# Kernel optimization log

Hardware: AMD Instinct MI355X
Metric: run time of the kernel (lower is better)

## Reference

```python
import jax, jax.numpy as jnp
from jax import lax
import numpy as np

GRID_SIZE = 8
MARGIN = 1.0
NUM_NEG = 16
SOS_NEG = 8
LOSS_LAMBDA = 1.0
B, N, C = 2, 512, 128
H = W = 128  # descriptor map; image is GRID_SIZE*H = 1024


def dist_matrix(a, b):
    # Euclidean cdist for 2-D points; exact 0 for identical rows (needed for <=1e-8 tests).
    d = a[:, :, None, :] - b[:, None, :, :]
    # distances only feed topk indices / boolean masks -> no grad path (matches torch)
    return lax.stop_gradient(jnp.sqrt(jnp.sum(d * d, axis=-1)))


def inv_sim_matrix(d1, d2):
    return 2.0 - 2.0 * jnp.einsum('bnc,bmc->bnm', d1, d2)


def inv_sim_vector(d1, d2):
    return 2.0 - 2.0 * jnp.sum(d1 * d2, axis=-1)


def make_coo_grid(h, w, gs, b):
    ys = gs * jnp.arange(h, dtype=jnp.float32) + gs / 2.0
    xs = gs * jnp.arange(w, dtype=jnp.float32) + gs / 2.0
    g = jnp.stack(jnp.meshgrid(ys, xs, indexing='ij'), axis=-1)  # H W 2 (y, x)
    return jnp.broadcast_to(g.reshape(1, h * w, 2), (b, h * w, 2))


def warp_points(p, Hm):
    xy = p[..., ::-1]  # (y,x) -> (x,y)
    ph = jnp.concatenate([xy, jnp.ones_like(xy[..., :1])], axis=-1)
    wp = jnp.einsum('bij,bmj->bmi', Hm, ph)
    wp = wp[..., :2] / (wp[..., 2:3] + 1e-8)
    return wp[..., ::-1]  # back to (y,x)


def sample_descriptors(desc, kp, gs):
    # bilinear sample of desc (B,C,H,W) at image-space keypoints (y,x), then L2-normalize
    b, c, h, w = desc.shape
    y = jnp.clip(kp[..., 0] / gs - 0.5, 0.0, h - 1.0)
    x = jnp.clip(kp[..., 1] / gs - 0.5, 0.0, w - 1.0)
    y0 = jnp.clip(jnp.floor(y), 0, h - 2).astype(jnp.int32)
    x0 = jnp.clip(jnp.floor(x), 0, w - 2).astype(jnp.int32)
    wy = (y - y0)[..., None]
    wx = (x - x0)[..., None]
    dmap = desc.transpose(0, 2, 3, 1).reshape(b, h * w, c)
    def g(yi, xi):
        idx = jnp.broadcast_to((yi * w + xi)[..., None], yi.shape + (c,))
        return jnp.take_along_axis(dmap, idx, axis=1)
    v = (g(y0, x0) * (1 - wy) * (1 - wx) + g(y0, x0 + 1) * (1 - wy) * wx
         + g(y0 + 1, x0) * wy * (1 - wx) + g(y0 + 1, x0 + 1) * wy * wx)
    return v / (jnp.linalg.norm(v, axis=-1, keepdims=True) + 1e-8)


def take2(coo, idx):
    # gather 2-D points: coo (B,M,2), idx (B,K) -> (B,K,2)
    return jnp.take_along_axis(coo, jnp.broadcast_to(idx[:, :, None], idx.shape + (2,)), axis=1)


def smallest_k(x, k):
    vals, ids = lax.top_k(-x, k)
    return -vals, ids


def setup_inputs() -> dict:
    key = jax.random.key(0)
    k1, k2, k3, k4, k5 = jax.random.split(key, 5)
    img = float(GRID_SIZE * H)
    kp1 = jax.random.uniform(k1, (B, N, 2), dtype=jnp.float32) * (img - 1.0)
    w_kp1 = jax.random.uniform(k2, (B, N, 2), dtype=jnp.float32) * (img - 1.0)
    d = jax.random.normal(k3, (B, N, C), dtype=jnp.float32)
    kp1_desc = d / jnp.linalg.norm(d, axis=-1, keepdims=True)
    desc2 = jax.random.normal(k4, (B, C, H, W), dtype=jnp.float32)
    homo12 = jnp.broadcast_to(jnp.eye(3, dtype=jnp.float32), (B, 3, 3)) \
        + 1e-3 * jax.random.normal(k5, (B, 3, 3), dtype=jnp.float32)
    return {'kp1': kp1, 'w_kp1': w_kp1, 'kp1_desc': kp1_desc, 'desc2': desc2, 'homo12': homo12}


def reference(kp1, w_kp1, kp1_desc, desc2, homo12):
    b, n, c = kp1_desc.shape
    _, _, h, w = desc2.shape
    hw = h * w
    gs = GRID_SIZE

    w_kp1_desc = sample_descriptors(desc2, w_kp1, gs)  # b n c
    pos = inv_sim_vector(kp1_desc, w_kp1_desc)  # b n
    pos = jnp.repeat(pos[:, :, None], NUM_NEG, axis=2).reshape(b, n * NUM_NEG)

    coo = make_coo_grid(h, w, gs, b)  # b hw 2
    kp1_cell_ids = smallest_k(dist_matrix(kp1, coo), 4)[1].reshape(b, 4 * n)
    kp1_cells = take2(coo, kp1_cell_ids)  # b 4n 2
    kp1_w_cells = warp_points(kp1_cells, homo12)
    kp1_w_cell_cell_ids = smallest_k(dist_matrix(kp1_w_cells, coo), 4)[1]  # b 4n 4

    bb = jnp.arange(b)[:, None, None]
    rr = jnp.arange(4 * n)[None, :, None]
    neigh = jnp.zeros((b, 4 * n, hw), jnp.float32).at[bb, rr, kp1_w_cell_cell_ids].set(1.0)
    neigh = neigh.reshape(b, n, 4, hw).sum(axis=2)  # b n hw

    desc2f = desc2.transpose(0, 2, 3, 1).reshape(b, hw, c)
    dsim = inv_sim_matrix(kp1_desc, desc2f) + neigh * 5.0
    neg = smallest_k(dsim, NUM_NEG)[0].reshape(b, n * NUM_NEG)
    fos = jnp.mean(jnp.maximum(pos - neg + MARGIN, 0.0) ** 2) * LOSS_LAMBDA

    cc = dist_matrix(kp1_cells, kp1_cells)  # b 4n 4n
    kp1_mask = (cc <= 1e-8).reshape(b, n, 4, n, 4).sum(-1).sum(2).astype(jnp.float32)  # b n n

    kp1_w_cell_cells = take2(coo, kp1_w_cell_cell_ids.reshape(b, 16 * n))  # b 16n 2
    w_ids = smallest_k(dist_matrix(w_kp1, coo), 4)[1].reshape(b, 4 * n)
    w_kp1_cells = take2(coo, w_ids)  # b 4n 2
    d4 = dist_matrix(kp1_w_cell_cells, w_kp1_cells)  # b 16n 4n
    w_kp1_mask = (d4 <= 1e-8).reshape(b, n, 4, 4, n, 4).sum(-1).sum(3).sum(2).astype(jnp.float32)

    k_sim = inv_sim_matrix(kp1_desc, kp1_desc) + kp1_mask * 5.0
    w_sim = inv_sim_matrix(w_kp1_desc, w_kp1_desc) + w_kp1_mask * 5.0
    k_neg_ids = smallest_k(k_sim, SOS_NEG)[1].reshape(b, n * SOS_NEG)
    w_neg_ids = smallest_k(w_sim, SOS_NEG)[1].reshape(b, n * SOS_NEG)

    def gatherC(x, idx):
        return jnp.take_along_axis(x, jnp.broadcast_to(idx[:, :, None], idx.shape + (c,)), axis=1)
    k_neg_desc = gatherC(kp1_desc, k_neg_ids)
    w_neg_desc = gatherC(w_kp1_desc, w_neg_ids)
    k_rep = jnp.repeat(kp1_desc[:, :, None, :], SOS_NEG, axis=2).reshape(b, n * SOS_NEG, c)
    w_rep = jnp.repeat(w_kp1_desc[:, :, None, :], SOS_NEG, axis=2).reshape(b, n * SOS_NEG, c)

    sos_v = inv_sim_vector(k_rep, k_neg_desc) - inv_sim_vector(w_rep, w_neg_desc)
    sos = jnp.mean(jnp.sqrt(jnp.sum((sos_v ** 2).reshape(b, n, SOS_NEG), axis=-1)))
    return (fos + sos) * LOSS_LAMBDA
```

## Files before the change

### kernel.cpp

```cpp
#include <hip/hip_runtime.h>
#include <climits>

#define B_ 2
#define N_ 512
#define C_ 128
#define H_ 128
#define W_ 128
#define HW_ (H_ * W_)
#define NUM_NEG_ 16
#define SOS_NEG_ 8
#define SCAP_ 128

typedef __attribute__((ext_vector_type(8))) short short8;
typedef __attribute__((ext_vector_type(4))) float f32x4;

__device__ inline unsigned int f2bf(float x) {
    unsigned int u = __float_as_uint(x);
    return (u + 0x7FFFu + ((u >> 16) & 1u)) >> 16;
}
__device__ inline float bf2f(unsigned int h) {
    return __uint_as_float(h << 16);
}

__device__ inline void nearest4(float y, float x, int out[4]) {
// ... 150 lines not shown
        s += __shfl_xor(s, 1);  s += __shfl_xor(s, 2);  s += __shfl_xor(s, 4);
        s += __shfl_xor(s, 8);  s += __shfl_xor(s, 16); s += __shfl_xor(s, 32);
        float inv = 1.0f / (sqrtf(s) + 1e-8f);
        float vn0 = v0 * inv, vn1 = v1 * inv;
        w_bf[(size_t)bn * C_ + l]      = (unsigned short)f2bf(vn0);
        w_bf[(size_t)bn * C_ + 64 + l] = (unsigned short)f2bf(vn1);
        float qd0 = kp1_desc[(size_t)bn * C_ + l];
        float qd1 = kp1_desc[(size_t)bn * C_ + 64 + l];
        float d = qd0 * vn0 + qd1 * vn1;
        d += __shfl_xor(d, 1);  d += __shfl_xor(d, 2);  d += __shfl_xor(d, 4);
        d += __shfl_xor(d, 8);  d += __shfl_xor(d, 16); d += __shfl_xor(d, 32);
        if (l == 0) pos[bn] = 2.0f - 2.0f * d;
    }
}

__global__ __launch_bounds__(512) void hqt_kb(
    const unsigned short* __restrict__ q_bf,
    const unsigned short* __restrict__ w_bf,
    const unsigned short* __restrict__ d2t,
    const int* __restrict__ cid4, const int* __restrict__ wid4,
    const int* __restrict__ wcc16,
    float* __restrict__ rowmax, float* __restrict__ psim) {
    int blk = blockIdx.x;
    int tid = threadIdx.x, w = tid >> 6, l = tid & 63;
    int l15 = l & 15, lg = l >> 4;
    if (blk < 256) {
        int b = blk >> 7;
        int rg = (blk >> 4) & 7;
        int cb = blk & 15;
        int rowbase = rg * 64;
        int colbase = cb * 1024 + w * 128;
        const unsigned short* qb = q_bf + (size_t)b * N_ * C_;
        const unsigned short* db = d2t + (size_t)b * HW_ * C_;
        short8 a[4][4];
#pragma unroll
        for (int rt = 0; rt < 4; ++rt)
#pragma unroll
            for (int ks = 0; ks < 4; ++ks)
                a[rt][ks] = *(const short8*)(qb + (size_t)(rowbase + rt * 16 + l15) * C_ + ks * 32 + lg * 8);
        f32x4 mx[4];
#pragma unroll
        for (int rt = 0; rt < 4; ++rt) mx[rt] = f32x4{-1e30f, -1e30f, -1e30f, -1e30f};
#pragma unroll
        for (int t = 0; t < 8; ++t) {
            const unsigned short* dp = db + (size_t)(colbase + t * 16 + l15) * C_ + lg * 8;
            short8 b0 = *(const short8*)(dp);
            short8 b1 = *(const short8*)(dp + 32);
            short8 b2 = *(const short8*)(dp + 64);
            short8 b3 = *(const short8*)(dp + 96);
#pragma unroll
            for (int rt = 0; rt < 4; ++rt) {
                f32x4 acc4 = {0.0f, 0.0f, 0.0f, 0.0f};
                acc4 = __builtin_amdgcn_mfma_f32_16x16x32_bf16(a[rt][0], b0, acc4, 0, 0, 0);
                acc4 = __builtin_amdgcn_mfma_f32_16x16x32_bf16(a[rt][1], b1, acc4, 0, 0, 0);
                acc4 = __builtin_amdgcn_mfma_f32_16x16x32_bf16(a[rt][2], b2, acc4, 0, 0, 0);
                acc4 = __builtin_amdgcn_mfma_f32_16x16x32_bf16(a[rt][3], b3, acc4, 0, 0, 0);
#pragma unroll
                for (int r = 0; r < 4; ++r) mx[rt][r] = fmaxf(mx[rt][r], acc4[r]);
            }
        }
#pragma unroll
        for (int rt = 0; rt < 4; ++rt)
#pragma unroll
            for (int r = 0; r < 4; ++r) {
                float v = mx[rt][r];
                v = fmaxf(v, __shfl_xor(v, 1));
                v = fmaxf(v, __shfl_xor(v, 2));
                v = fmaxf(v, __shfl_xor(v, 4));
                v = fmaxf(v, __shfl_xor(v, 8));
                mx[rt][r] = v;
            }
        if (l15 == 0) {
            int chunk = cb * 8 + w;
#pragma unroll
            for (int rt = 0; rt < 4; ++rt)
#pragma unroll
                for (int r = 0; r < 4; ++r) {
                    int rowg = b * N_ + rowbase + rt * 16 + lg * 4 + r;
                    rowmax[(size_t)rowg * 128 + chunk] = mx[rt][r];
                }
        }
    } else {
        int blk2 = blk - 256;
        int mat = blk2 >> 6;
        int b = (blk2 >> 5) & 1;
        int r0 = (blk2 & 31) * 16;
        const unsigned short* src = (mat ? w_bf : q_bf) + (size_t)b * N_ * C_;

        __shared__ int s_colids[N_][4];
        __shared__ int s_rowcc[16][16];
        {
            const int4* gsrc = (const int4*)((mat ? wid4 : cid4) + b * N_ * 4);
            ((int4*)s_colids)[tid] = gsrc[tid];
            if (tid < 256)
                ((int*)s_rowcc)[tid] = wcc16[(b * N_ + r0) * 16 + tid];
        }
        short8 a0 = *(const short8*)(src + (size_t)(r0 + l15) * C_ + lg * 8);
        short8 a1 = *(const short8*)(src + (size_t)(r0 + l15) * C_ + 32 + lg * 8);
        short8 a2 = *(const short8*)(src + (size_t)(r0 + l15) * C_ + 64 + lg * 8);
        short8 a3 = *(const short8*)(src + (size_t)(r0 + l15) * C_ + 96 + lg * 8);
        __syncthreads();

        int4 rowc[4];
        int rcc[4][16];
#pragma unroll
        for (int r = 0; r < 4; ++r) {
            rowc[r] = *(const int4*)(&s_colids[r0 + lg * 4 + r][0]);
            if (mat == 1) {
#pragma unroll
                for (int i = 0; i < 16; ++i) rcc[r][i] = s_rowcc[lg * 4 + r][i];
            }
        }

        float* prow = psim + ((size_t)(mat * B_ + b) * N_) * N_;
#pragma unroll
        for (int t = 0; t < 4; ++t) {
            int col0 = w * 64 + t * 16;
            const unsigned short* dp = src + (size_t)(col0 + l15) * C_ + lg * 8;
            short8 b0 = *(const short8*)(dp);
            short8 b1 = *(const short8*)(dp + 32);
            short8 b2 = *(const short8*)(dp + 64);
            short8 b3 = *(const short8*)(dp + 96);
            f32x4 acc4 = {0.0f, 0.0f, 0.0f, 0.0f};
            acc4 = __builtin_amdgcn_mfma_f32_16x16x32_bf16(a0, b0, acc4, 0, 0, 0);
            acc4 = __builtin_amdgcn_mfma_f32_16x16x32_bf16(a1, b1, acc4, 0, 0, 0);
            acc4 = __builtin_amdgcn_mfma_f32_16x16x32_bf16(a2, b2, acc4, 0, 0, 0);
            acc4 = __builtin_amdgcn_mfma_f32_16x16x32_bf16(a3, b3, acc4, 0, 0, 0);
            int mycol = col0 + l15;
            int4 cc = *(const int4*)(&s_colids[mycol][0]);
#pragma unroll
            for (int r = 0; r < 4; ++r) {
                int cnt = 0;
                if (mat == 0) {
#pragma unroll
                    for (int j = 0; j < 4; ++j) {
                        int u = (j == 0) ? rowc[r].x : (j == 1) ? rowc[r].y
                              : (j == 2) ? rowc[r].z : rowc[r].w;
                        cnt += (u == cc.x) + (u == cc.y) + (u == cc.z) + (u == cc.w);
                    }
                } else {
#pragma unroll
                    for (int i = 0; i < 16; ++i) {
                        int u = rcc[r][i];
                        cnt += (u == cc.x) + (u == cc.y) + (u == cc.z) + (u == cc.w);
                    }
                }
                float key = acc4[r] - 2.5f * (float)cnt;
                prow[(size_t)(r0 + lg * 4 + r) * N_ + mycol] = key;
            }
        }
    }
}

__global__ __launch_bounds__(256) void hqt_k3b(
    const float* __restrict__ rowmax, float* __restrict__ t32) {
    int w = threadIdx.x >> 6, l = threadIdx.x & 63;
    int row = blockIdx.x * 4 + w;
    const float* rm = rowmax + (size_t)row * 128;
    float v = fmaxf(rm[l], rm[64 + l]);
    float t = -1e30f;
#pragma unroll 1
    for (int it = 0; it < 32; ++it) {
        float m = v;
        m = fmaxf(m, __shfl_xor(m, 1));
        m = fmaxf(m, __shfl_xor(m, 2));
        m = fmaxf(m, __shfl_xor(m, 4));
        m = fmaxf(m, __shfl_xor(m, 8));
        m = fmaxf(m, __shfl_xor(m, 16));
        m = fmaxf(m, __shfl_xor(m, 32));
        v = (v == m) ? -1e30f : v;
        t = m;
    }
    if (l == 0) t32[row] = t;
}

__global__ __launch_bounds__(512) void hqt_kc(
    const unsigned short* __restrict__ q_bf,
    const unsigned short* __restrict__ d2t,
    const float* __restrict__ t32,
    int* __restrict__ scnt, float2* __restrict__ sbuf) {
    int blk = blockIdx.x;
    int b = blk >> 7;
    int rg = (blk >> 4) & 7;
    int cb = blk & 15;
    int tid = threadIdx.x, w = tid >> 6, l = tid & 63;
    int l15 = l & 15, lg = l >> 4;
    int rowbase = rg * 64;
    int colbase = cb * 1024 + w * 128;
    const unsigned short* qb = q_bf + (size_t)b * N_ * C_;
    const unsigned short* db = d2t + (size_t)b * HW_ * C_;
    short8 a[4][4];
#pragma unroll
    for (int rt = 0; rt < 4; ++rt)
#pragma unroll
        for (int ks = 0; ks < 4; ++ks)
            a[rt][ks] = *(const short8*)(qb + (size_t)(rowbase + rt * 16 + l15) * C_ + ks * 32 + lg * 8);
    float tl[4][4];
#pragma unroll
    for (int rt = 0; rt < 4; ++rt)
#pragma unroll
        for (int r = 0; r < 4; ++r)
            tl[rt][r] = t32[b * N_ + rowbase + rt * 16 + lg * 4 + r];
#pragma unroll
    for (int t = 0; t < 8; ++t) {
        const unsigned short* dp = db + (size_t)(colbase + t * 16 + l15) * C_ + lg * 8;
        short8 b0 = *(const short8*)(dp);
        short8 b1 = *(const short8*)(dp + 32);
        short8 b2 = *(const short8*)(dp + 64);
        short8 b3 = *(const short8*)(dp + 96);
#pragma unroll
        for (int rt = 0; rt < 4; ++rt) {
            f32x4 acc4 = {0.0f, 0.0f, 0.0f, 0.0f};
            acc4 = __builtin_amdgcn_mfma_f32_16x16x32_bf16(a[rt][0], b0, acc4, 0, 0, 0);
            acc4 = __builtin_amdgcn_mfma_f32_16x16x32_bf16(a[rt][1], b1, acc4, 0, 0, 0);
            acc4 = __builtin_amdgcn_mfma_f32_16x16x32_bf16(a[rt][2], b2, acc4, 0, 0, 0);
            acc4 = __builtin_amdgcn_mfma_f32_16x16x32_bf16(a[rt][3], b3, acc4, 0, 0, 0);
#pragma unroll
            for (int r = 0; r < 4; ++r) {
                float d = acc4[r];
                if (d >= tl[rt][r]) {
                    int rowg = b * N_ + rowbase + rt * 16 + lg * 4 + r;
                    int idx = atomicAdd(scnt + rowg, 1);
                    if (idx < SCAP_) {
                        float2 e;
                        e.x = d;
                        e.y = __int_as_float(colbase + t * 16 + l15);
                        sbuf[(size_t)rowg * SCAP_ + idx] = e;
                    }
                }
            }
        }
    }
}

__device__ inline void insert8_vi(float (&av)[8], int (&ai)[8], float v, int id) {
    bool le = (v < av[7]) || (v == av[7] && id < ai[7]);
    if (!le) return;
#pragma unroll
    for (int k = 0; k < 8; ++k) {
        float ov = av[k]; int oi = ai[k];
        bool sm = (v < ov) || (v == ov && id < oi);
        av[k] = sm ? v : ov;  ai[k] = sm ? id : oi;
        v = sm ? ov : v;      id = sm ? oi : id;
    }
}

__device__ inline void bitonic8_pairs(float (&av)[8], int (&ai)[8]) {
#pragma unroll
    for (int dd = 0; dd < 3; ++dd) {
        const int d = 4 >> dd;
#pragma unroll
        for (int i = 0; i < 8; ++i) {
            if ((i & d) == 0) {
                bool sw = (av[i + d] < av[i]) ||
                          (av[i + d] == av[i] && ai[i + d] < ai[i]);
                float tv = av[i]; int ti = ai[i];
                av[i]     = sw ? av[i + d] : av[i];
                ai[i]     = sw ? ai[i + d] : ai[i];
                av[i + d] = sw ? tv : av[i + d];
                ai[i + d] = sw ? ti : ai[i + d];
            }
        }
    }
}

__device__ inline void wave_merge8(float (&av)[8], int (&ai)[8], int l) {
#pragma unroll
    for (int step = 32; step >= 1; step >>= 1) {
        float bv[8]; int bi2[8];
#pragma unroll
        for (int i = 0; i < 8; ++i) {
            bv[i]  = __shfl(av[7 - i], (l + step) & 63);
            bi2[i] = __shfl(ai[7 - i], (l + step) & 63);
        }
        bool upd = l < step;
#pragma unroll
        for (int i = 0; i < 8; ++i) {
            bool sm = (bv[i] < av[i]) || (bv[i] == av[i] && bi2[i] < ai[i]);
            if (upd && sm) { av[i] = bv[i]; ai[i] = bi2[i]; }
        }
        bitonic8_pairs(av, ai);
    }
}

__global__ __launch_bounds__(256) void hqt_kd(
    const unsigned short* __restrict__ q_bf,
    const unsigned short* __restrict__ d2t,
    const unsigned int* __restrict__ marked,
    const int* __restrict__ scnt, const float2* __restrict__ sbuf,
    const float* __restrict__ pos, const float* __restrict__ psim,
    const int* __restrict__ cid4, const int* __restrict__ wid4,
    const int* __restrict__ wcc16, float* __restrict__ acc,
    float* __restrict__ out) {
    int blk = blockIdx.x;
    int w = threadIdx.x >> 6, l = threadIdx.x & 63;
    if (blk < 256) {
        int row = blk * 4 + w;
        int b = row >> 9;
        int sc = scnt[row]; if (sc > SCAP_) sc = SCAP_;
        float k0 = -1e30f, k1 = -1e30f, k2c = -1e30f;
        int c0 = -1, c1 = -1;
        if (l < sc) {
            float2 e = sbuf[(size_t)row * SCAP_ + l];
            k0 = e.x; c0 = __float_as_int(e.y);
        }
        if (64 + l < sc) {
            float2 e = sbuf[(size_t)row * SCAP_ + 64 + l];
            k1 = e.x; c1 = __float_as_int(e.y);
        }
#pragma unroll
        for (int i = 0; i < 16; ++i) {
            unsigned int mv = marked[row * 16 + i];
            int id = (int)(mv & 0xFFFFu);
            if (c0 == id) k0 = -1e30f;
            if (c1 == id) k1 = -1e30f;
        }
        {
            int mi = l >> 2, cq = l & 3;
            unsigned int mv = marked[row * 16 + mi];
            bool valid = (mv != 0xFFFFFFFFu);
            int col = valid ? (int)(mv & 0xFFFFu) : 0;
            int cnt = (int)(mv >> 16);
            const unsigned short* qp = q_bf + (size_t)row * C_ + cq * 32;
            const unsigned short* dp = d2t + ((size_t)b * HW_ + col) * C_ + cq * 32;
            float dot = 0.0f;
#pragma unroll
            for (int u = 0; u < 4; ++u) {
                short8 qv = *(const short8*)(qp + u * 8);
                short8 dv = *(const short8*)(dp + u * 8);
#pragma unroll
                for (int e = 0; e < 8; ++e)
                    dot = fmaf(bf2f((unsigned short)qv[e]), bf2f((unsigned short)dv[e]), dot);
            }
            dot += __shfl_xor(dot, 1);
            dot += __shfl_xor(dot, 2);
            k2c = (valid && cq == 0) ? (dot - 2.5f * (float)cnt) : -1e30f;
        }
        float pos_r = pos[row];
        float sum = 0.0f;
#pragma unroll 1
        for (int it = 0; it < 16; ++it) {
            float v = fmaxf(k0, fmaxf(k1, k2c));
            float m = v;
            m = fmaxf(m, __shfl_xor(m, 1));
            m = fmaxf(m, __shfl_xor(m, 2));
            m = fmaxf(m, __shfl_xor(m, 4));
            m = fmaxf(m, __shfl_xor(m, 8));
            m = fmaxf(m, __shfl_xor(m, 16));
            m = fmaxf(m, __shfl_xor(m, 32));
            unsigned long long b0 = __ballot(k0 == m);
            if (b0) {
                if (l == __ffsll(b0) - 1) k0 = -1e30f;
            } else {
                unsigned long long b1 = __ballot(k1 == m);
                if (b1) {
                    if (l == __ffsll(b1) - 1) k1 = -1e30f;
                } else {
                    unsigned long long b2 = __ballot(k2c == m);
                    if (l == __ffsll(b2) - 1) k2c = -1e30f;
                }
            }
            float h = pos_r + 2.0f * m - 1.0f;
            h = fmaxf(h, 0.0f);
            sum += h * h;
        }
        if (l == 0) atomicAdd(acc + 0, sum);
    } else {
        int rowg = (blk - 256) * 4 + w;
        int b = rowg >> 9;
        int row = rowg & 511;

        __shared__ float s_kv[4][8], s_wv[4][8];
        __shared__ int   s_ki[4][8], s_wi[4][8];

        float kv[8]; int ki[8];
#pragma unroll
        for (int i = 0; i < 8; ++i) { kv[i] = 1e30f; ki[i] = INT_MAX; }
        {
            const float* pk = psim + ((size_t)(0 * B_ + b) * N_ + row) * N_;
            float4 u0 = ((const float4*)pk)[l * 2];
            float4 u1 = ((const float4*)pk)[l * 2 + 1];
            insert8_vi(kv, ki, -u0.x, l * 8 + 0);
            insert8_vi(kv, ki, -u0.y, l * 8 + 1);
            insert8_vi(kv, ki, -u0.z, l * 8 + 2);
            insert8_vi(kv, ki, -u0.w, l * 8 + 3);
            insert8_vi(kv, ki, -u1.x, l * 8 + 4);
            insert8_vi(kv, ki, -u1.y, l * 8 + 5);
            insert8_vi(kv, ki, -u1.z, l * 8 + 6);
            insert8_vi(kv, ki, -u1.w, l * 8 + 7);
        }
        wave_merge8(kv, ki, l);
        if (l == 0) {
#pragma unroll
            for (int i = 0; i < 8; ++i) { s_kv[w][i] = -kv[i]; s_ki[w][i] = ki[i]; }
        }

        float wv[8]; int wi[8];
#pragma unroll
        for (int i = 0; i < 8; ++i) { wv[i] = 1e30f; wi[i] = INT_MAX; }
        {
            const float* pw = psim + ((size_t)(1 * B_ + b) * N_ + row) * N_;
            float4 u0 = ((const float4*)pw)[l * 2];
            float4 u1 = ((const float4*)pw)[l * 2 + 1];
            insert8_vi(wv, wi, -u0.x, l * 8 + 0);
            insert8_vi(wv, wi, -u0.y, l * 8 + 1);
            insert8_vi(wv, wi, -u0.z, l * 8 + 2);
            insert8_vi(wv, wi, -u0.w, l * 8 + 3);
            insert8_vi(wv, wi, -u1.x, l * 8 + 4);
            insert8_vi(wv, wi, -u1.y, l * 8 + 5);
            insert8_vi(wv, wi, -u1.z, l * 8 + 6);
            insert8_vi(wv, wi, -u1.w, l * 8 + 7);
        }
        wave_merge8(wv, wi, l);
        if (l == 0) {
#pragma unroll
            for (int i = 0; i < 8; ++i) { s_wv[w][i] = -wv[i]; s_wi[w][i] = wi[i]; }
        }

        if (l < 8) {
            int kidx = s_ki[w][l]; float kkey = s_kv[w][l];
            int widx = s_wi[w][l]; float wkey = s_wv[w][l];
            const int4* cb  = (const int4*)(cid4 + b * N_ * 4);
            const int4* wb4 = (const int4*)(wid4 + b * N_ * 4);
            int4 rc = cb[row];
            int4 mc = cb[kidx];
            int cntK = 0;
#pragma unroll
            for (int j = 0; j < 4; ++j) {
                int u = (j == 0) ? rc.x : (j == 1) ? rc.y : (j == 2) ? rc.z : rc.w;
                cntK += (u == mc.x) + (u == mc.y) + (u == mc.z) + (u == mc.w);
            }
            int4 mw = wb4[widx];
            int cntW = 0;
            const int4* rcc = (const int4*)(wcc16 + (b * N_ + row) * 16);
#pragma unroll
            for (int uq = 0; uq < 4; ++uq) {
                int4 rr = rcc[uq];
                cntW += (rr.x == mw.x) + (rr.x == mw.y) + (rr.x == mw.z) + (rr.x == mw.w);
                cntW += (rr.y == mw.x) + (rr.y == mw.y) + (rr.y == mw.z) + (rr.y == mw.w);
                cntW += (rr.z == mw.x) + (rr.z == mw.y) + (rr.z == mw.z) + (rr.z == mw.w);
                cntW += (rr.w == mw.x) + (rr.w == mw.y) + (rr.w == mw.z) + (rr.w == mw.w);
            }
            float dotK = kkey + 2.5f * (float)cntK;
            float dotW = wkey + 2.5f * (float)cntW;
            float t2 = 2.0f * (dotW - dotK);
            float sq = t2 * t2;
            sq += __shfl_xor(sq, 1);
            sq += __shfl_xor(sq, 2);
            sq += __shfl_xor(sq, 4);
            if (l == 0) atomicAdd(acc + 1, sqrtf(sq));
        }
    }
    __syncthreads();
    if (threadIdx.x == 0) {
        __threadfence();
        unsigned int t = atomicAdd((unsigned int*)(acc + 2), 1u);
        if (t == 511u) {
            float a0 = atomicAdd(acc + 0, 0.0f);
            float a1 = atomicAdd(acc + 1, 0.0f);
            out[0] = a0 * (1.0f / (float)(B_ * N_ * NUM_NEG_))
                   + a1 * (1.0f / (float)(B_ * N_));
        }
    }
}

__global__ void hqt_k1_cells(const float* __restrict__ kp1,
                             const float* __restrict__ w_kp1,
                             const float* __restrict__ homo,
                             int* __restrict__ cid4,
                             int* __restrict__ wcc16,
                             int* __restrict__ wid4) {
    int t = blockIdx.x * blockDim.x + threadIdx.x;
    if (t >= B_ * N_) return;
    int b = t / N_;
    float ky = kp1[2 * t], kx = kp1[2 * t + 1];
    int ids[4];
    nearest4(ky, kx, ids);
    const float* Hb = homo + 9 * b;
    float h00 = Hb[0], h01 = Hb[1], h02 = Hb[2];
    float h10 = Hb[3], h11 = Hb[4], h12 = Hb[5];
    float h20 = Hb[6], h21 = Hb[7], h22 = Hb[8];
#pragma unroll
    for (int i = 0; i < 4; ++i) {
        int id = ids[i];
        cid4[4 * t + i] = id;
        float cy = 8.0f * (id >> 7) + 4.0f;
        float cx = 8.0f * (id & 127) + 4.0f;
        float X = cx, Y = cy;
        float wz = h20 * X + h21 * Y + h22;
        float inv = 1.0f / (wz + 1e-8f);
        float wy = (h10 * X + h11 * Y + h12) * inv;
        float wx = (h00 * X + h01 * Y + h02) * inv;
        int wids[4];
        nearest4(wy, wx, wids);
#pragma unroll
        for (int j = 0; j < 4; ++j) wcc16[16 * t + 4 * i + j] = wids[j];
    }
    float zy = w_kp1[2 * t], zx = w_kp1[2 * t + 1];
    int wi4[4];
    nearest4(zy, zx, wi4);
#pragma unroll
    for (int j = 0; j < 4; ++j) wid4[4 * t + j] = wi4[j];
}

__global__ __launch_bounds__(128) void hqt_k2_sample_f32(
    const float* __restrict__ w_kp1, const float* __restrict__ desc2,
    const float* __restrict__ kp1_desc, float* __restrict__ w_desc,
    float* __restrict__ pos) {
    int bn = blockIdx.x;
    int b = bn / N_;
    int c = threadIdx.x;
    float ky = w_kp1[2 * bn], kx = w_kp1[2 * bn + 1];
    float y = fminf(fmaxf(ky * 0.125f - 0.5f, 0.0f), (float)(H_ - 1));
    float x = fminf(fmaxf(kx * 0.125f - 0.5f, 0.0f), (float)(W_ - 1));
    int y0 = (int)floorf(y); if (y0 > H_ - 2) y0 = H_ - 2;
    int x0 = (int)floorf(x); if (x0 > W_ - 2) x0 = W_ - 2;
    float wy = y - (float)y0, wx = x - (float)x0;
    const float* dB = desc2 + ((size_t)b * C_ + c) * HW_;
    int i00 = y0 * W_ + x0;
    float v = dB[i00]          * (1.0f - wy) * (1.0f - wx)
            + dB[i00 + 1]      * (1.0f - wy) * wx
            + dB[i00 + W_]     * wy * (1.0f - wx)
            + dB[i00 + W_ + 1] * wy * wx;
    __shared__ float red[128];
    red[c] = v * v;
    __syncthreads();
    for (int s = 64; s > 0; s >>= 1) {
        if (c < s) red[c] += red[c + s];
        __syncthreads();
    }
    float nrm = sqrtf(red[0]);
    __syncthreads();
    float vn = v / (nrm + 1e-8f);
    w_desc[(size_t)bn * C_ + c] = vn;
    float qd = kp1_desc[(size_t)bn * C_ + c];
    red[c] = qd * vn;
    __syncthreads();
    for (int s = 64; s > 0; s >>= 1) {
        if (c < s) red[c] += red[c + s];
        __syncthreads();
    }
    if (c == 0) pos[bn] = 2.0f - 2.0f * red[0];
}

__device__ inline void bitonic16_asc(float (&a)[16]) {
#pragma unroll
    for (int dd = 0; dd < 4; ++dd) {
        const int d = 8 >> dd;
#pragma unroll
        for (int i = 0; i < 16; ++i) {
            if ((i & d) == 0) {
                float lo = fminf(a[i], a[i + d]);
                float hi = fmaxf(a[i], a[i + d]);
                a[i] = lo; a[i + d] = hi;
            }
        }
    }
}

#define T3 512
#define R3 4
__global__ __launch_bounds__(T3) void hqt_k3_dsim(
    const float* __restrict__ desc2, const float* __restrict__ kp1_desc,
    const int* __restrict__ wcc16, const float* __restrict__ pos,
    float* __restrict__ acc) {
    const int nb = N_ / R3;
    int b = blockIdx.x / nb;
    int n0 = (blockIdx.x % nb) * R3;
    int tid = threadIdx.x;
    __shared__ float qT[C_][R3];
    __shared__ int ids_s[R3][16];
    {
        int r = tid & 3, c = tid >> 2;
        qT[c][r] = kp1_desc[(size_t)(b * N_ + n0 + r) * C_ + c];
    }
    if (tid < R3 * 16)
        ids_s[tid >> 4][tid & 15] = wcc16[(b * N_ + n0) * 16 + tid];
    __syncthreads();

    float top[R3][16];
#pragma unroll
    for (int r = 0; r < R3; ++r)
#pragma unroll
        for (int k = 0; k < 16; ++k) top[r][k] = 1e30f;

    const float* d2b = desc2 + (size_t)b * C_ * HW_;
#pragma unroll 1
    for (int g = 0; g < HW_ / (T3 * 4); ++g) {
        int j0 = (g * T3 + tid) * 4;
        float4 A0 = {0, 0, 0, 0}, A1 = {0, 0, 0, 0}, A2 = {0, 0, 0, 0}, A3 = {0, 0, 0, 0};
        for (int c = 0; c < C_; ++c) {
            float4 d = *reinterpret_cast<const float4*>(d2b + (size_t)c * HW_ + j0);
            float4 qv = *reinterpret_cast<const float4*>(&qT[c][0]);
            A0.x = fmaf(qv.x, d.x, A0.x); A0.y = fmaf(qv.x, d.y, A0.y);
            A0.z = fmaf(qv.x, d.z, A0.z); A0.w = fmaf(qv.x, d.w, A0.w);
            A1.x = fmaf(qv.y, d.x, A1.x); A1.y = fmaf(qv.y, d.y, A1.y);
            A1.z = fmaf(qv.y, d.z, A1.z); A1.w = fmaf(qv.y, d.w, A1.w);
            A2.x = fmaf(qv.z, d.x, A2.x); A2.y = fmaf(qv.z, d.y, A2.y);
            A2.z = fmaf(qv.z, d.z, A2.z); A2.w = fmaf(qv.z, d.w, A2.w);
            A3.x = fmaf(qv.w, d.x, A3.x); A3.y = fmaf(qv.w, d.y, A3.y);
            A3.z = fmaf(qv.w, d.z, A3.z); A3.w = fmaf(qv.w, d.w, A3.w);
        }
#pragma unroll
        for (int r = 0; r < R3; ++r) {
            float dots[4];
            dots[0] = (r == 0) ? A0.x : (r == 1) ? A1.x : (r == 2) ? A2.x : A3.x;
            dots[1] = (r == 0) ? A0.y : (r == 1) ? A1.y : (r == 2) ? A2.y : A3.y;
            dots[2] = (r == 0) ? A0.z : (r == 1) ? A1.z : (r == 2) ? A2.z : A3.z;
            dots[3] = (r == 0) ? A0.w : (r == 1) ? A1.w : (r == 2) ? A2.w : A3.w;
#pragma unroll
            for (int cc = 0; cc < 4; ++cc) {
                int j = j0 + cc;
                int cnt = 0;
#pragma unroll
                for (int i = 0; i < 16; ++i) cnt += (ids_s[r][i] == j) ? 1 : 0;
                float v = 2.0f - 2.0f * dots[cc] + 5.0f * (float)cnt;
                if (v < top[r][15]) {
#pragma unroll
                    for (int k = 0; k < 16; ++k) {
                        float o = top[r][k];
                        bool sm = v < o;
                        top[r][k] = sm ? v : o;
                        v = sm ? o : v;
                    }
                }
            }
        }
    }

    __shared__ float mv[T3][17];
#pragma unroll
    for (int r = 0; r < R3; ++r) {
        float a[16];
#pragma unroll
        for (int k = 0; k < 16; ++k) { a[k] = top[r][k]; mv[tid][k] = a[k]; }
        __syncthreads();
        for (int step = T3 / 2; step >= 1; step >>= 1) {
            if (tid < step) {
#pragma unroll
                for (int i = 0; i < 16; ++i)
                    a[i] = fminf(a[i], mv[tid + step][15 - i]);
                bitonic16_asc(a);
#pragma unroll
                for (int i = 0; i < 16; ++i) mv[tid][i] = a[i];
            }
            __syncthreads();
        }
        if (tid == 0) {
            float p = pos[b * N_ + n0 + r];
            float s = 0.0f;
#pragma unroll
            for (int k = 0; k < 16; ++k) {
                float xv = p - a[k] + 1.0f;
                xv = fmaxf(xv, 0.0f);
                s += xv * xv;
            }
            atomicAdd(acc + 0, s);
        }
        __syncthreads();
    }
}

__global__ __launch_bounds__(64) void hqt_k4_sos(
    const float* __restrict__ kp1_desc, const float* __restrict__ w_desc,
    const int* __restrict__ cid4, const int* __restrict__ wcc16,
    const int* __restrict__ wid4, float* __restrict__ acc) {
    int bn = blockIdx.x;
    int b = bn / N_;
    int lane = threadIdx.x;
    __shared__ float qk[C_], qw[C_];
    for (int c = lane; c < C_; c += 64) {
        qk[c] = kp1_desc[(size_t)bn * C_ + c];
        qw[c] = w_desc[(size_t)bn * C_ + c];
    }
    __syncthreads();
    int nk[4];
#pragma unroll
    for (int i = 0; i < 4; ++i) nk[i] = cid4[4 * bn + i];
    int nw[16];
#pragma unroll
    for (int i = 0; i < 16; ++i) nw[i] = wcc16[16 * bn + i];

    float kv[8], wv[8]; int ki[8], wi[8];
#pragma unroll
    for (int k = 0; k < 8; ++k) {
        kv[k] = 1e30f; wv[k] = 1e30f; ki[k] = INT_MAX; wi[k] = INT_MAX;
    }
    const float* kb = kp1_desc + (size_t)b * N_ * C_;
    const float* wb = w_desc + (size_t)b * N_ * C_;
    for (int tt = 0; tt < 8; ++tt) {
        int m = lane * 8 + tt;
        const float* rk = kb + (size_t)m * C_;
        const float* rw = wb + (size_t)m * C_;
        float dk = 0.0f, dw = 0.0f;
        for (int c = 0; c < C_; c += 4) {
            float4 xk = *(const float4*)(rk + c);
            float4 xw = *(const float4*)(rw + c);
            dk += qk[c] * xk.x + qk[c + 1] * xk.y + qk[c + 2] * xk.z + qk[c + 3] * xk.w;
            dw += qw[c] * xw.x + qw[c + 1] * xw.y + qw[c + 2] * xw.z + qw[c + 3] * xw.w;
        }
        int4 mc = *(const int4*)(cid4 + 4 * (b * N_ + m));
        int ck = 0;
#pragma unroll
        for (int i = 0; i < 4; ++i) {
            int u = nk[i];
            ck += (u == mc.x) + (u == mc.y) + (u == mc.z) + (u == mc.w);
        }
        int4 mw = *(const int4*)(wid4 + 4 * (b * N_ + m));
        int cw = 0;
#pragma unroll
        for (int i = 0; i < 16; ++i) {
            int u = nw[i];
            cw += (u == mw.x) + (u == mw.y) + (u == mw.z) + (u == mw.w);
        }
        float vk = 2.0f - 2.0f * dk + 5.0f * (float)ck;
        float vw2 = 2.0f - 2.0f * dw + 5.0f * (float)cw;
        insert8_vi(kv, ki, vk, m);
        insert8_vi(wv, wi, vw2, m);
    }

    __shared__ float mvs[64][9];
    __shared__ int mis[64][9];
    __shared__ int fk[8], fw[8];

#pragma unroll
    for (int i = 0; i < 8; ++i) { mvs[lane][i] = kv[i]; mis[lane][i] = ki[i]; }
    __syncthreads();
    for (int step = 32; step >= 1; step >>= 1) {
        if (lane < step) {
            float bv[8]; int bix[8];
#pragma unroll
            for (int i = 0; i < 8; ++i) {
                bv[i] = mvs[lane + step][7 - i];
                bix[i] = mis[lane + step][7 - i];
            }
#pragma unroll
            for (int i = 0; i < 8; ++i) {
                bool ta = (kv[i] < bv[i]) || (kv[i] == bv[i] && ki[i] < bix[i]);
                kv[i] = ta ? kv[i] : bv[i];
                ki[i] = ta ? ki[i] : bix[i];
            }
            bitonic8_pairs(kv, ki);
#pragma unroll
            for (int i = 0; i < 8; ++i) { mvs[lane][i] = kv[i]; mis[lane][i] = ki[i]; }
        }
        __syncthreads();
    }
    if (lane < 8) fk[lane] = mis[0][lane];
    __syncthreads();

#pragma unroll
    for (int i = 0; i < 8; ++i) { mvs[lane][i] = wv[i]; mis[lane][i] = wi[i]; }
    __syncthreads();
    for (int step = 32; step >= 1; step >>= 1) {
        if (lane < step) {
            float bv[8]; int bix[8];
#pragma unroll
            for (int i = 0; i < 8; ++i) {
                bv[i] = mvs[lane + step][7 - i];
                bix[i] = mis[lane + step][7 - i];
            }
#pragma unroll
            for (int i = 0; i < 8; ++i) {
                bool ta = (wv[i] < bv[i]) || (wv[i] == bv[i] && wi[i] < bix[i]);
                wv[i] = ta ? wv[i] : bv[i];
                wi[i] = ta ? wi[i] : bix[i];
            }
            bitonic8_pairs(wv, wi);
#pragma unroll
            for (int i = 0; i < 8; ++i) { mvs[lane][i] = wv[i]; mis[lane][i] = wi[i]; }
        }
        __syncthreads();
    }
    if (lane < 8) fw[lane] = mis[0][lane];
    __syncthreads();

    int s = lane >> 3, p = lane & 7;
    const float* rk = kb + (size_t)fk[s] * C_;
    const float* rw = wb + (size_t)fw[s] * C_;
    float dk = 0.0f, dw = 0.0f;
    for (int c = p; c < C_; c += 8) {
        dk += qk[c] * rk[c];
        dw += qw[c] * rw[c];
    }
    dk += __shfl_xor(dk, 1); dk += __shfl_xor(dk, 2); dk += __shfl_xor(dk, 4);
    dw += __shfl_xor(dw, 1); dw += __shfl_xor(dw, 2); dw += __shfl_xor(dw, 4);
    __shared__ float tsq[8];
    if (p == 0) {
        float t2 = 2.0f * (dw - dk);
        tsq[s] = t2 * t2;
    }
    __syncthreads();
    if (lane == 0) {
        float s8 = 0.0f;
#pragma unroll
        for (int i = 0; i < 8; ++i) s8 += tsq[i];
        atomicAdd(acc + 1, sqrtf(s8));
    }
}

__global__ void hqt_k5_final(const float* __restrict__ acc, float* __restrict__ out) {
    if (threadIdx.x == 0 && blockIdx.x == 0) {
        out[0] = acc[0] * (1.0f / (float)(B_ * N_ * NUM_NEG_))
               + acc[1] * (1.0f / (float)(B_ * N_));
    }
}

extern "C" void kernel_launch(void* const* d_in, const int* in_sizes, int n_in,
                              void* d_out, int out_size, void* d_ws, size_t ws_size,
                              hipStream_t stream) {
    const float* kp1      = (const float*)d_in[0];
    const float* w_kp1    = (const float*)d_in[1];
    const float* kp1_desc = (const float*)d_in[2];
    const float* desc2    = (const float*)d_in[3];
    const float* homo     = (const float*)d_in[4];
    float* out = (float*)d_out;

    char* p = (char*)d_ws;
    auto alloc = [&](size_t bytes) {
        char* r = p;
        p += (bytes + 255) & ~(size_t)255;
        return r;
    };
    float*          pos    = (float*)alloc((size_t)B_ * N_ * 4);
    int*            cid4   = (int*)alloc((size_t)B_ * N_ * 4 * 4);
    int*            wid4   = (int*)alloc((size_t)B_ * N_ * 4 * 4);
    int*            wcc16  = (int*)alloc((size_t)B_ * N_ * 16 * 4);
    unsigned int*   marked = (unsigned int*)alloc((size_t)B_ * N_ * 16 * 4);
    float*          acc    = (float*)alloc(64);
    unsigned short* q_bf   = (unsigned short*)alloc((size_t)B_ * N_ * C_ * 2);
    unsigned short* w_bf   = (unsigned short*)alloc((size_t)B_ * N_ * C_ * 2);
    unsigned short* d2t    = (unsigned short*)alloc((size_t)B_ * HW_ * C_ * 2);
    float*          psim   = (float*)alloc((size_t)2 * B_ * N_ * N_ * 4);
    float*          rowmax = (float*)alloc((size_t)B_ * N_ * 128 * 4);
    float*          t32    = (float*)alloc((size_t)B_ * N_ * 4);
    int*            scnt   = (int*)alloc((size_t)B_ * N_ * 4);
    float2*         sbuf   = (float2*)alloc((size_t)B_ * N_ * SCAP_ * 8);
    size_t need = (size_t)(p - (char*)d_ws);

    if (ws_size >= need) {
        hqt_ka<<<1413, 256, 0, stream>>>(desc2, kp1_desc, kp1, w_kp1, homo,
                                         d2t, q_bf, w_bf, pos, cid4, wcc16,
                                         wid4, marked, scnt, acc);
        hqt_kb<<<384, 512, 0, stream>>>(q_bf, w_bf, d2t, cid4, wid4, wcc16,
                                        rowmax, psim);
        hqt_k3b<<<256, 256, 0, stream>>>(rowmax, t32);
        hqt_kc<<<256, 512, 0, stream>>>(q_bf, d2t, t32, scnt, sbuf);
        hqt_kd<<<512, 256, 0, stream>>>(q_bf, d2t, marked, scnt, sbuf, pos,
                                        psim, cid4, wid4, wcc16, acc, out);
    } else {
        float* w_desc0 = (float*)d_ws;
        float* pos0    = w_desc0 + (size_t)B_ * N_ * C_;
        int*   cid40   = (int*)(pos0 + B_ * N_);
        int*   wid40   = cid40 + B_ * N_ * 4;
        int*   wcc160  = wid40 + B_ * N_ * 4;
        float* acc0    = (float*)(wcc160 + B_ * N_ * 16);
        hipMemsetAsync(acc0, 0, 2 * sizeof(float), stream);
        hqt_k1_cells<<<(B_ * N_ + 255) / 256, 256, 0, stream>>>(
            kp1, w_kp1, homo, cid40, wcc160, wid40);
        hqt_k2_sample_f32<<<B_ * N_, 128, 0, stream>>>(w_kp1, desc2, kp1_desc,
                                                       w_desc0, pos0);
        hqt_k3_dsim<<<B_ * (N_ / R3), T3, 0, stream>>>(desc2, kp1_desc, wcc160,
                                                       pos0, acc0);
        hqt_k4_sos<<<B_ * N_, 64, 0, stream>>>(kp1_desc, w_desc0, cid40,
                                               wcc160, wid40, acc0);
        hqt_k5_final<<<1, 1, 0, stream>>>(acc0, out);
    }
}
```

Before: 135.0 us.

## Fuse row-threshold kernel into candidate kernel and use rank-based top-k selection

The separate threshold kernel (32 iterative wave max-reductions per row) is removed, and each candidate-scan block now computes the 32nd-largest rowmax value itself through a parallel rank count over the row held in LDS. In the final kernel, the 16-iteration serial max/ballot extraction for the hinge loss is replaced by one-pass rank counting over 144 keys in shared memory. The SOS top-8 selection switches from per-lane insertion sort plus shuffle merge to a top-2-per-lane threshold, atomic compaction and ranking. This saves one launch and removes long serial shuffle chains, at the cost of redundant threshold computation in every column block (16x per row group) and extra LDS and barriers.

```diff
diff --git a/kernel.cpp b/kernel.cpp
--- a/kernel.cpp
+++ b/kernel.cpp
@@ -326,32 +326,10 @@
     }
 }
 
-__global__ __launch_bounds__(256) void hqt_k3b(
-    const float* __restrict__ rowmax, float* __restrict__ t32) {
-    int w = threadIdx.x >> 6, l = threadIdx.x & 63;
-    int row = blockIdx.x * 4 + w;
-    const float* rm = rowmax + (size_t)row * 128;
-    float v = fmaxf(rm[l], rm[64 + l]);
-    float t = -1e30f;
-#pragma unroll 1
-    for (int it = 0; it < 32; ++it) {
-        float m = v;
-        m = fmaxf(m, __shfl_xor(m, 1));
-        m = fmaxf(m, __shfl_xor(m, 2));
-        m = fmaxf(m, __shfl_xor(m, 4));
-        m = fmaxf(m, __shfl_xor(m, 8));
-        m = fmaxf(m, __shfl_xor(m, 16));
-        m = fmaxf(m, __shfl_xor(m, 32));
-        v = (v == m) ? -1e30f : v;
-        t = m;
-    }
-    if (l == 0) t32[row] = t;
-}
-
 __global__ __launch_bounds__(512) void hqt_kc(
     const unsigned short* __restrict__ q_bf,
     const unsigned short* __restrict__ d2t,
-    const float* __restrict__ t32,
+    const float* __restrict__ rowmax,
     int* __restrict__ scnt, float2* __restrict__ sbuf) {
     int blk = blockIdx.x;
     int b = blk >> 7;
@@ -361,6 +339,42 @@
     int l15 = l & 15, lg = l >> 4;
     int rowbase = rg * 64;
     int colbase = cb * 1024 + w * 128;
+
+    __shared__ float rm[64][128];
+    __shared__ float t32_l[64];
+    {
+        int row = tid >> 3, g = tid & 7;
+        const float* src = rowmax + ((size_t)(b * N_ + rowbase + row) * 128 + g * 16);
+        float4* dst = (float4*)&rm[row][g * 16];
+        dst[0] = ((const float4*)src)[0];
+        dst[1] = ((const float4*)src)[1];
+        dst[2] = ((const float4*)src)[2];
+        dst[3] = ((const float4*)src)[3];
+    }
+    __syncthreads();
+    {
+        int row = tid >> 3, g = tid & 7;
+        float cand[16];
+        int rk[16];
+#pragma unroll
+        for (int k = 0; k < 16; ++k) { cand[k] = rm[row][g * 16 + k]; rk[k] = 0; }
+        for (int j = 0; j < 128; j += 4) {
+            float4 kk = *(const float4*)&rm[row][j];
+#pragma unroll
+            for (int e = 0; e < 4; ++e) {
+                float key = (e == 0) ? kk.x : (e == 1) ? kk.y : (e == 2) ? kk.z : kk.w;
+                int jj = j + e;
+#pragma unroll
+                for (int k = 0; k < 16; ++k)
+                    rk[k] += (key > cand[k]) || (key == cand[k] && jj < g * 16 + k);
+            }
+        }
+#pragma unroll
+        for (int k = 0; k < 16; ++k)
+            if (rk[k] == 31) t32_l[row] = cand[k];
+    }
+    __syncthreads();
+
     const unsigned short* qb = q_bf + (size_t)b * N_ * C_;
     const unsigned short* db = d2t + (size_t)b * HW_ * C_;
     short8 a[4][4];
@@ -374,7 +388,7 @@
     for (int rt = 0; rt < 4; ++rt)
 #pragma unroll
         for (int r = 0; r < 4; ++r)
-            tl[rt][r] = t32[b * N_ + rowbase + rt * 16 + lg * 4 + r];
+            tl[rt][r] = t32_l[rt * 16 + lg * 4 + r];
 #pragma unroll
     for (int t = 0; t < 8; ++t) {
         const unsigned short* dp = db + (size_t)(colbase + t * 16 + l15) * C_ + lg * 8;
@@ -407,56 +421,6 @@
     }
 }
 
-__device__ inline void insert8_vi(float (&av)[8], int (&ai)[8], float v, int id) {
-    bool le = (v < av[7]) || (v == av[7] && id < ai[7]);
-    if (!le) return;
-#pragma unroll
-    for (int k = 0; k < 8; ++k) {
-        float ov = av[k]; int oi = ai[k];
-        bool sm = (v < ov) || (v == ov && id < oi);
-        av[k] = sm ? v : ov;  ai[k] = sm ? id : oi;
-        v = sm ? ov : v;      id = sm ? oi : id;
-    }
-}
-
-__device__ inline void bitonic8_pairs(float (&av)[8], int (&ai)[8]) {
-#pragma unroll
-    for (int dd = 0; dd < 3; ++dd) {
-        const int d = 4 >> dd;
-#pragma unroll
-        for (int i = 0; i < 8; ++i) {
-            if ((i & d) == 0) {
-                bool sw = (av[i + d] < av[i]) ||
-                          (av[i + d] == av[i] && ai[i + d] < ai[i]);
-                float tv = av[i]; int ti = ai[i];
-                av[i]     = sw ? av[i + d] : av[i];
-                ai[i]     = sw ? ai[i + d] : ai[i];
-                av[i + d] = sw ? tv : av[i + d];
-                ai[i + d] = sw ? ti : ai[i + d];
-            }
-        }
-    }
-}
-
-__device__ inline void wave_merge8(float (&av)[8], int (&ai)[8], int l) {
-#pragma unroll
-    for (int step = 32; step >= 1; step >>= 1) {
-        float bv[8]; int bi2[8];
-#pragma unroll
-        for (int i = 0; i < 8; ++i) {
-            bv[i]  = __shfl(av[7 - i], (l + step) & 63);
-            bi2[i] = __shfl(ai[7 - i], (l + step) & 63);
-        }
-        bool upd = l < step;
-#pragma unroll
-        for (int i = 0; i < 8; ++i) {
-            bool sm = (bv[i] < av[i]) || (bv[i] == av[i] && bi2[i] < ai[i]);
-            if (upd && sm) { av[i] = bv[i]; ai[i] = bi2[i]; }
-        }
-        bitonic8_pairs(av, ai);
-    }
-}
-
 __global__ __launch_bounds__(256) void hqt_kd(
     const unsigned short* __restrict__ q_bf,
     const unsigned short* __restrict__ d2t,
@@ -469,10 +433,11 @@
     int blk = blockIdx.x;
     int w = threadIdx.x >> 6, l = threadIdx.x & 63;
     if (blk < 256) {
+        __shared__ float keys[4][160];
         int row = blk * 4 + w;
         int b = row >> 9;
         int sc = scnt[row]; if (sc > SCAP_) sc = SCAP_;
-        float k0 = -1e30f, k1 = -1e30f, k2c = -1e30f;
+        float k0 = -1e30f, k1 = -1e30f;
         int c0 = -1, c1 = -1;
         if (l < sc) {
             float2 e = sbuf[(size_t)row * SCAP_ + l];
@@ -489,8 +454,10 @@
             if (c0 == id) k0 = -1e30f;
             if (c1 == id) k1 = -1e30f;
         }
+        float k2c = -1e30f;
+        int mi = l >> 2;
         {
-            int mi = l >> 2, cq = l & 3;
+            int cq = l & 3;
             unsigned int mv = marked[row * 16 + mi];
             bool valid = (mv != 0xFFFFFFFFu);
             int col = valid ? (int)(mv & 0xFFFFu) : 0;
@@ -508,116 +475,126 @@
             }
             dot += __shfl_xor(dot, 1);
             dot += __shfl_xor(dot, 2);
-            k2c = (valid && cq == 0) ? (dot - 2.5f * (float)cnt) : -1e30f;
+            k2c = valid ? (dot - 2.5f * (float)cnt) : -1e30f;
+            keys[w][l] = k0;
+            keys[w][64 + l] = k1;
+            if (cq == 0) keys[w][128 + mi] = k2c;
+            if (l < 16) keys[w][144 + l] = -1e30f;
+        }
+        __syncthreads();
+        float cC = (l < 16) ? keys[w][128 + l] : -1e30f;
+        int idxC = 128 + l;
+        int r0 = 0, r1 = 0, r2 = 0;
+        for (int j = 0; j < 144; j += 4) {
+            float4 kk = *(const float4*)&keys[w][j];
+#pragma unroll
+            for (int e = 0; e < 4; ++e) {
+                float key = (e == 0) ? kk.x : (e == 1) ? kk.y : (e == 2) ? kk.z : kk.w;
+                int jj = j + e;
+                r0 += (key > k0) || (key == k0 && jj < l);
+                r1 += (key > k1) || (key == k1 && jj < 64 + l);
+                r2 += (key > cC) || (key == cC && jj < idxC);
+            }
         }
         float pos_r = pos[row];
         float sum = 0.0f;
-#pragma unroll 1
-        for (int it = 0; it < 16; ++it) {
-            float v = fmaxf(k0, fmaxf(k1, k2c));
-            float m = v;
-            m = fmaxf(m, __shfl_xor(m, 1));
-            m = fmaxf(m, __shfl_xor(m, 2));
-            m = fmaxf(m, __shfl_xor(m, 4));
-            m = fmaxf(m, __shfl_xor(m, 8));
-            m = fmaxf(m, __shfl_xor(m, 16));
-            m = fmaxf(m, __shfl_xor(m, 32));
-            unsigned long long b0 = __ballot(k0 == m);
-            if (b0) {
-                if (l == __ffsll(b0) - 1) k0 = -1e30f;
-            } else {
-                unsigned long long b1 = __ballot(k1 == m);
-                if (b1) {
-                    if (l == __ffsll(b1) - 1) k1 = -1e30f;
-                } else {
-                    unsigned long long b2 = __ballot(k2c == m);
-                    if (l == __ffsll(b2) - 1) k2c = -1e30f;
-                }
-            }
-            float h = pos_r + 2.0f * m - 1.0f;
-            h = fmaxf(h, 0.0f);
-            sum += h * h;
-        }
+        if (r0 < 16) { float h = fmaxf(pos_r + 2.0f * k0 - 1.0f, 0.0f); sum += h * h; }
+        if (r1 < 16) { float h = fmaxf(pos_r + 2.0f * k1 - 1.0f, 0.0f); sum += h * h; }
+        if (r2 < 16) { float h = fmaxf(pos_r + 2.0f * cC - 1.0f, 0.0f); sum += h * h; }
+        sum += __shfl_xor(sum, 1);  sum += __shfl_xor(sum, 2);
+        sum += __shfl_xor(sum, 4);  sum += __shfl_xor(sum, 8);
+        sum += __shfl_xor(sum, 16); sum += __shfl_xor(sum, 32);
         if (l == 0) atomicAdd(acc + 0, sum);
     } else {
+        __shared__ float cand[4][128];
+        __shared__ float sval[4][64];
+        __shared__ int   scol[4][64];
+        __shared__ int   cnt_l[4];
+        __shared__ float tpp[4];
+        __shared__ float sel[4][2][8];
         int rowg = (blk - 256) * 4 + w;
         int b = rowg >> 9;
         int row = rowg & 511;
-
-        __shared__ float s_kv[4][8], s_wv[4][8];
-        __shared__ int   s_ki[4][8], s_wi[4][8];
-
-        float kv[8]; int ki[8];
-#pragma unroll
-        for (int i = 0; i < 8; ++i) { kv[i] = 1e30f; ki[i] = INT_MAX; }
-        {
-            const float* pk = psim + ((size_t)(0 * B_ + b) * N_ + row) * N_;
-            float4 u0 = ((const float4*)pk)[l * 2];
-            float4 u1 = ((const float4*)pk)[l * 2 + 1];
-            insert8_vi(kv, ki, -u0.x, l * 8 + 0);
-            insert8_vi(kv, ki, -u0.y, l * 8 + 1);
-            insert8_vi(kv, ki, -u0.z, l * 8 + 2);
-            insert8_vi(kv, ki, -u0.w, l * 8 + 3);
-            insert8_vi(kv, ki, -u1.x, l * 8 + 4);
-            insert8_vi(kv, ki, -u1.y, l * 8 + 5);
-            insert8_vi(kv, ki, -u1.z, l * 8 + 6);
-            insert8_vi(kv, ki, -u1.w, l * 8 + 7);
-        }
-        wave_merge8(kv, ki, l);
-        if (l == 0) {
-#pragma unroll
-            for (int i = 0; i < 8; ++i) { s_kv[w][i] = -kv[i]; s_ki[w][i] = ki[i]; }
-        }
-
-        float wv[8]; int wi[8];
-#pragma unroll
-        for (int i = 0; i < 8; ++i) { wv[i] = 1e30f; wi[i] = INT_MAX; }
-        {
-            const float* pw = psim + ((size_t)(1 * B_ + b) * N_ + row) * N_;
-            float4 u0 = ((const float4*)pw)[l * 2];
-            float4 u1 = ((const float4*)pw)[l * 2 + 1];
-            insert8_vi(wv, wi, -u0.x, l * 8 + 0);
-            insert8_vi(wv, wi, -u0.y, l * 8 + 1);
-            insert8_vi(wv, wi, -u0.z, l * 8 + 2);
-            insert8_vi(wv, wi, -u0.w, l * 8 + 3);
-            insert8_vi(wv, wi, -u1.x, l * 8 + 4);
-            insert8_vi(wv, wi, -u1.y, l * 8 + 5);
-            insert8_vi(wv, wi, -u1.z, l * 8 + 6);
-            insert8_vi(wv, wi, -u1.w, l * 8 + 7);
-        }
-        wave_merge8(wv, wi, l);
-        if (l == 0) {
-#pragma unroll
-            for (int i = 0; i < 8; ++i) { s_wv[w][i] = -wv[i]; s_wi[w][i] = wi[i]; }
-        }
-
+#pragma unroll 1
+        for (int mat = 0; mat < 2; ++mat) {
+            const float* pr = psim + ((size_t)(mat * B_ + b) * N_ + row) * N_;
+            float4 u0 = ((const float4*)pr)[l * 2];
+            float4 u1 = ((const float4*)pr)[l * 2 + 1];
+            float k[8] = {u0.x, u0.y, u0.z, u0.w, u1.x, u1.y, u1.z, u1.w};
+            float m1 = -1e30f, m2 = -1e30f;
+#pragma unroll
+            for (int i = 0; i < 8; ++i) {
+                float v = k[i];
+                bool g1 = v > m1;
+                m2 = g1 ? m1 : fmaxf(m2, v);
+                m1 = g1 ? v : m1;
+            }
+            if (l == 0) cnt_l[w] = 0;
+            cand[w][l] = m1;
+            cand[w][64 + l] = m2;
+            __syncthreads();
+            int rA = 0, rB = 0;
+            for (int j = 0; j < 128; j += 4) {
+                float4 cc = *(const float4*)&cand[w][j];
+#pragma unroll
+                for (int e = 0; e < 4; ++e) {
+                    float cv = (e == 0) ? cc.x : (e == 1) ? cc.y : (e == 2) ? cc.z : cc.w;
+                    int jj = j + e;
+                    rA += (cv > m1) || (cv == m1 && jj < l);
+                    rB += (cv > m2) || (cv == m2 && jj < 64 + l);
+                }
+            }
+            if (rA == 7) tpp[w] = m1;
+            if (rB == 7) tpp[w] = m2;
+            __syncthreads();
+            float t8 = tpp[w];
+#pragma unroll
+            for (int i = 0; i < 8; ++i) {
+                if (k[i] >= t8) {
+                    int s = atomicAdd(&cnt_l[w], 1);
+                    if (s < 64) { sval[w][s] = k[i]; scol[w][s] = l * 8 + i; }
+                }
+            }
+            __syncthreads();
+            int cnt = cnt_l[w]; if (cnt > 64) cnt = 64;
+            float sv = (l < cnt) ? sval[w][l] : -1e30f;
+            int   scm = (l < cnt) ? scol[w][l] : INT_MAX;
+            int r = 0;
+            for (int j = 0; j < cnt; ++j) {
+                float vj = sval[w][j];
+                int cj = scol[w][j];
+                r += (vj > sv) || (vj == sv && cj < scm);
+            }
+            if (l < cnt && r < 8) {
+                int cntm = 0;
+                if (mat == 0) {
+                    const int4* cb4 = (const int4*)(cid4 + b * N_ * 4);
+                    int4 rc = cb4[row];
+                    int4 mc = cb4[scm];
+#pragma unroll
+                    for (int j = 0; j < 4; ++j) {
+                        int u = (j == 0) ? rc.x : (j == 1) ? rc.y : (j == 2) ? rc.z : rc.w;
+                        cntm += (u == mc.x) + (u == mc.y) + (u == mc.z) + (u == mc.w);
+                    }
+                } else {
+                    const int4* wb4 = (const int4*)(wid4 + b * N_ * 4);
+                    int4 mw = wb4[scm];
+                    const int4* rcc = (const int4*)(wcc16 + (b * N_ + row) * 16);
+#pragma unroll
+                    for (int uq = 0; uq < 4; ++uq) {
+                        int4 rr = rcc[uq];
+                        cntm += (rr.x == mw.x) + (rr.x == mw.y) + (rr.x == mw.z) + (rr.x == mw.w);
+                        cntm += (rr.y == mw.x) + (rr.y == mw.y) + (rr.y == mw.z) + (rr.y == mw.w);
+                        cntm += (rr.z == mw.x) + (rr.z == mw.y) + (rr.z == mw.z) + (rr.z == mw.w);
+                        cntm += (rr.w == mw.x) + (rr.w == mw.y) + (rr.w == mw.z) + (rr.w == mw.w);
+                    }
+                }
+                sel[w][mat][r] = sv + 2.5f * (float)cntm;
+            }
+            __syncthreads();
+        }
         if (l < 8) {
-            int kidx = s_ki[w][l]; float kkey = s_kv[w][l];
-            int widx = s_wi[w][l]; float wkey = s_wv[w][l];
-            const int4* cb  = (const int4*)(cid4 + b * N_ * 4);
-            const int4* wb4 = (const int4*)(wid4 + b * N_ * 4);
-            int4 rc = cb[row];
-            int4 mc = cb[kidx];
-            int cntK = 0;
-#pragma unroll
-            for (int j = 0; j < 4; ++j) {
-                int u = (j == 0) ? rc.x : (j == 1) ? rc.y : (j == 2) ? rc.z : rc.w;
-                cntK += (u == mc.x) + (u == mc.y) + (u == mc.z) + (u == mc.w);
-            }
-            int4 mw = wb4[widx];
-            int cntW = 0;
-            const int4* rcc = (const int4*)(wcc16 + (b * N_ + row) * 16);
-#pragma unroll
-            for (int uq = 0; uq < 4; ++uq) {
-                int4 rr = rcc[uq];
-                cntW += (rr.x == mw.x) + (rr.x == mw.y) + (rr.x == mw.z) + (rr.x == mw.w);
-                cntW += (rr.y == mw.x) + (rr.y == mw.y) + (rr.y == mw.z) + (rr.y == mw.w);
-                cntW += (rr.z == mw.x) + (rr.z == mw.y) + (rr.z == mw.z) + (rr.z == mw.w);
-                cntW += (rr.w == mw.x) + (rr.w == mw.y) + (rr.w == mw.z) + (rr.w == mw.w);
-            }
-            float dotK = kkey + 2.5f * (float)cntK;
-            float dotW = wkey + 2.5f * (float)cntW;
-            float t2 = 2.0f * (dotW - dotK);
+            float t2 = 2.0f * (sel[w][1][l] - sel[w][0][l]);
             float sq = t2 * t2;
             sq += __shfl_xor(sq, 1);
             sq += __shfl_xor(sq, 2);
@@ -717,6 +694,37 @@
     if (c == 0) pos[bn] = 2.0f - 2.0f * red[0];
 }
 
+__device__ inline void insert8_vi(float (&av)[8], int (&ai)[8], float v, int id) {
+    bool le = (v < av[7]) || (v == av[7] && id < ai[7]);
+    if (!le) return;
+#pragma unroll
+    for (int k = 0; k < 8; ++k) {
+        float ov = av[k]; int oi = ai[k];
+        bool sm = (v < ov) || (v == ov && id < oi);
+        av[k] = sm ? v : ov;  ai[k] = sm ? id : oi;
+        v = sm ? ov : v;      id = sm ? oi : id;
+    }
+}
+
+__device__ inline void bitonic8_pairs(float (&av)[8], int (&ai)[8]) {
+#pragma unroll
+    for (int dd = 0; dd < 3; ++dd) {
+        const int d = 4 >> dd;
+#pragma unroll
+        for (int i = 0; i < 8; ++i) {
+            if ((i & d) == 0) {
+                bool sw = (av[i + d] < av[i]) ||
+                          (av[i + d] == av[i] && ai[i + d] < ai[i]);
+                float tv = av[i]; int ti = ai[i];
+                av[i]     = sw ? av[i + d] : av[i];
+                ai[i]     = sw ? ai[i + d] : ai[i];
+                av[i + d] = sw ? tv : av[i + d];
+                ai[i + d] = sw ? ti : ai[i + d];
+            }
+        }
+    }
+}
+
 __device__ inline void bitonic16_asc(float (&a)[16]) {
 #pragma unroll
     for (int dd = 0; dd < 4; ++dd) {
@@ -1007,7 +1015,6 @@
     unsigned short* d2t    = (unsigned short*)alloc((size_t)B_ * HW_ * C_ * 2);
     float*          psim   = (float*)alloc((size_t)2 * B_ * N_ * N_ * 4);
     float*          rowmax = (float*)alloc((size_t)B_ * N_ * 128 * 4);
-    float*          t32    = (float*)alloc((size_t)B_ * N_ * 4);
     int*            scnt   = (int*)alloc((size_t)B_ * N_ * 4);
     float2*         sbuf   = (float2*)alloc((size_t)B_ * N_ * SCAP_ * 8);
     size_t need = (size_t)(p - (char*)d_ws);
@@ -1018,8 +1025,7 @@
                                          wid4, marked, scnt, acc);
         hqt_kb<<<384, 512, 0, stream>>>(q_bf, w_bf, d2t, cid4, wid4, wcc16,
                                         rowmax, psim);
-        hqt_k3b<<<256, 256, 0, stream>>>(rowmax, t32);
-        hqt_kc<<<256, 512, 0, stream>>>(q_bf, d2t, t32, scnt, sbuf);
+        hqt_kc<<<256, 512, 0, stream>>>(q_bf, d2t, rowmax, scnt, sbuf);
         hqt_kd<<<512, 256, 0, stream>>>(q_bf, d2t, marked, scnt, sbuf, pos,
                                         psim, cid4, wid4, wcc16, acc, out);
     } else {
```

New measurement: 208.1 us. 1.54x slower.
